# Optimization experiments

Hardware: AMD Instinct MI355X
Metric: run time of the kernel (lower is better)

The kernel has to match this reference:

```python
import jax, jax.numpy as jnp
import numpy as np
from jax import lax

B, T, D, H = 4096, 256, 18, 32


def setup_inputs() -> dict:
    key = jax.random.key(0)
    ks = jax.random.split(key, 9)
    s = 1.0 / np.sqrt(H)  # PyTorch LSTM init scale
    return {
        "batch": jax.random.normal(ks[0], (B, T, D), dtype=jnp.float32),
        "W_ih": jax.random.normal(ks[1], (4 * H, D), dtype=jnp.float32) * s,
        "W_hh": jax.random.normal(ks[2], (4 * H, H), dtype=jnp.float32) * s,
        "b_ih": jax.random.normal(ks[3], (4 * H,), dtype=jnp.float32) * s,
        "b_hh": jax.random.normal(ks[4], (4 * H,), dtype=jnp.float32) * s,
        "W1": jax.random.normal(ks[5], (512, H * T), dtype=jnp.float32) * 0.02,
        "b1": jax.random.normal(ks[6], (512,), dtype=jnp.float32) * 0.02,
        "W2": jax.random.normal(ks[7], (1, 512), dtype=jnp.float32) * 0.02,
        "b2": jax.random.normal(ks[8], (1,), dtype=jnp.float32) * 0.02,
    }


def _lstm(batch, W_ih, W_hh, b_ih, b_hh):
    b, t, _ = batch.shape
    h = batch.dtype.type
    # Precompute input projections for all timesteps: [B, T, 4H]
    x_proj = jnp.einsum('bti,gi->btg', batch, W_ih) + b_ih + b_hh
    W_hh_T = W_hh.T  # [H, 4H]

    def step(carry, xp):
        h_prev, c_prev = carry
        gates = xp + h_prev @ W_hh_T  # [B, 4H]
        i, f, g, o = jnp.split(gates, 4, axis=-1)  # PyTorch gate order i,f,g,o
        i = jax.nn.sigmoid(i)
        f = jax.nn.sigmoid(f)
        g = jnp.tanh(g)
        o = jax.nn.sigmoid(o)
        c = f * c_prev + i * g
        h_new = o * jnp.tanh(c)
        return (h_new, c), h_new

    h0 = jnp.zeros((b, H), dtype=batch.dtype)
    c0 = jnp.zeros((b, H), dtype=batch.dtype)
    _, hs = lax.scan(step, (h0, c0), x_proj.transpose(1, 0, 2))  # hs: [T, B, H]
    return hs.transpose(1, 0, 2)  # [B, T, H]


def reference(batch, W_ih, W_hh, b_ih, b_hh, W1, b1, W2, b2):
    hs = _lstm(batch, W_ih, W_hh, b_ih, b_hh)            # [B, T, H]
    flat = hs.reshape(hs.shape[0], -1)                   # [B, T*H]
    hid = jax.nn.relu(flat @ W1.T + b1)                  # [B, 512]
    return hid @ W2.T + b2                               # [B, 1]
```

## Files before the change

### kernel.cpp

```cpp
#include <hip/hip_runtime.h>
#include <hip/hip_bf16.h>
#include <stdint.h>

typedef float f32x4 __attribute__((ext_vector_type(4)));
typedef _Float16 half8 __attribute__((ext_vector_type(8)));

#define B_ 4096
#define T_ 256
#define D_ 18
#define H_ 32
#define GK 8192
#define GN 512
#define KSPLIT 4
#define SLOT 520

__device__ __forceinline__ float fsig(float x) {
  float e = __builtin_amdgcn_exp2f(-1.442695041f * x);
  return __builtin_amdgcn_rcpf(1.0f + e);
}
__device__ __forceinline__ void ldsbar() {
  asm volatile("s_waitcnt lgkmcnt(0)\n\ts_barrier" ::: "memory");
}

__global__ __launch_bounds__(256) void cvtw1_kernel(const float* __restrict__ w1,
                                                    unsigned short* __restrict__ dst) {
  int i = blockIdx.x * 256 + threadIdx.x;
  float4 v = ((const float4*)w1)[i];
  unsigned short a = __builtin_bit_cast(unsigned short, (_Float16)v.x);
  unsigned short b = __builtin_bit_cast(unsigned short, (_Float16)v.y);
  unsigned short c = __builtin_bit_cast(unsigned short, (_Float16)v.z);
  unsigned short d = __builtin_bit_cast(unsigned short, (_Float16)v.w);
  uint2 o; o.x = (unsigned)a | ((unsigned)b << 16); o.y = (unsigned)c | ((unsigned)d << 16);
  ((uint2*)dst)[i] = o;
}

__global__ __launch_bounds__(512) void lstm_kernel(
    const float* __restrict__ batch, const float* __restrict__ W_ih,
    const float* __restrict__ W_hh, const float* __restrict__ b_ih,
    const float* __restrict__ b_hh, _Float16* __restrict__ hs) {
  __shared__ _Float16 hist[16 * SLOT];
  __shared__ _Float16 xs[2 * 4096];

  const int tid = (int)threadIdx.x;
  const int lane = tid & 63;
  const int w = tid >> 6;
  const int lq = lane >> 4;
  const int lr = lane & 15;
  const int b0 = (int)blockIdx.x * 16;

  half8 wx, wh;
  {
    int grow = (lr & 3) * 32 + w * 4 + (lr >> 2);
#pragma unroll
    for (int j = 0; j < 8; ++j) {
      int k = lq * 8 + j;
      wx[j] = (k < D_) ? (_Float16)W_ih[grow * D_ + k] : (_Float16)0.0f;
      wh[j] = (_Float16)W_hh[grow * H_ + k];
    }
  }
  f32x4 bias4;
#pragma unroll
  for (int r = 0; r < 4; ++r) {
    int g = r * 32 + w * 4 + lq;
    bias4[r] = b_ih[g] + b_hh[g];
  }

  const int rdo = lr * 32 + ((lq ^ ((lr >> 1) & 3)) << 3);
  const int kcol = w * 4 + lq;
  const int wro = lr * 32 + ((((kcol >> 3) ^ ((lr >> 1) & 3))) << 3) + (kcol & 7);

  const int fe = tid >> 5;
  const int fs = (tid >> 2) & 7;
  const int fg = tid & 3;
  const int fl_rd = fs * SLOT + fe * 32 + ((fg ^ ((fe >> 1) & 3)) << 3);
  _Float16* fl_wp = hs + (size_t)(b0 + fe) * GK + fs * H_ + fg * 8;

  const int e0 = tid / 36, q0 = tid - e0 * 36;
  const int i1 = tid + 512;
  const int e1 = i1 / 36, q1 = i1 - e1 * 36;
  const float* xld0 = batch + (size_t)(b0 + e0) * (T_ * D_) + q0 * 4;
  const float* xld1 = batch + (size_t)(b0 + e1) * (T_ * D_) + q1 * 4;
  float4 xv0, xv1;

#define XLOAD(tb)                                                              \
  do {                                                                         \
    xv0 = *(const float4*)(xld0 + (tb) * 144);                                 \
    if (tid < 64) xv1 = *(const float4*)(xld1 + (tb) * 144);                   \
  } while (0)

#define XPUT(E, Q, V, buf)                                                     \
  do {                                                                         \
    int swz_ = ((E) >> 1) & 3;                                                 \
    _Pragma("unroll") for (int j = 0; j < 4; ++j) {                            \
      int f_ = (Q) * 4 + j;                                                    \
      int to_ = (f_ * 57) >> 10;                          \
      int d_ = f_ - to_ * 18;                                                  \
      float val_ = (j == 0) ? (V).x : (j == 1) ? (V).y : (j == 2) ? (V).z : (V).w; \
      xs[(buf) * 4096 + to_ * 512 + (E) * 32 + (((d_ >> 3) ^ swz_) << 3) + (d_ & 7)] = \
          (_Float16)val_;                                                      \
    }                                                                          \
  } while (0)

#define XSTORE(buf)                                                            \
  do {                                                                         \
    XPUT(e0, q0, xv0, buf);                                                    \
    if (tid < 64) XPUT(e1, q1, xv1, buf);                                      \
  } while (0)

#define STEP(tt, AXC, PRE)                                                     \
  do {                                                                         \
    _Float16* hrd = ((tt) == 0 ? po + 7 * SLOT : pr + ((tt)-1) * SLOT);        \
    half8 hf = *(const half8*)&hrd[rdo];                                       \
    f32x4 acc = __builtin_amdgcn_mfma_f32_16x16x32_f16(wh, hf, AXC, 0, 0, 0);  \
    PRE;                                                                       \
    float ei = __builtin_amdgcn_exp2f(-1.442695041f * acc[0]);                 \
    float eg = __builtin_amdgcn_exp2f(-2.885390082f * acc[2]);                 \
    float ig = (1.0f - eg) *                                                   \
               __builtin_amdgcn_rcpf((1.0f + ei) * (1.0f + eg));               \
    float fv = fsig(acc[1]);                                                   \
    c = fmaf(fv, c, ig);                                                       \
    float eo = __builtin_amdgcn_exp2f(-1.442695041f * acc[3]);                 \
    float ec = __builtin_amdgcn_exp2f(-2.885390082f * c);                      \
    float h = (1.0f - ec) *                                                    \
              __builtin_amdgcn_rcpf((1.0f + eo) * (1.0f + ec));                \
    pr[(tt)*SLOT + wro] = (_Float16)h;                                         \
    ldsbar();                                                                  \
  } while (0)

  XLOAD(0);
  for (int i = tid; i < 16 * SLOT; i += 512) hist[i] = (_Float16)0.0f;
  for (int i = tid; i < 8192; i += 512) xs[i] = (_Float16)0.0f;
  ldsbar();
  XSTORE(0);
  XLOAD(1);
  ldsbar();

  float c = 0.0f;
  for (int blk = 0; blk < 32; ++blk) {
    const int p = blk & 1;
    _Float16* pr = hist + p * (8 * SLOT);
    _Float16* po = hist + (p ^ 1) * (8 * SLOT);
    const int xo = p * 4096;

    half8 xq[8];
#pragma unroll
    for (int j = 0; j < 8; ++j) xq[j] = *(const half8*)&xs[xo + j * 512 + rdo];
    f32x4 ax0, ax1;
    ax0 = __builtin_amdgcn_mfma_f32_16x16x32_f16(wx, xq[0], bias4, 0, 0, 0);

    STEP(0, ax0, ax1 = __builtin_amdgcn_mfma_f32_16x16x32_f16(wx, xq[1], bias4, 0, 0, 0));
    STEP(1, ax1, ax0 = __builtin_amdgcn_mfma_f32_16x16x32_f16(wx, xq[2], bias4, 0, 0, 0));
    STEP(2, ax0, ax1 = __builtin_amdgcn_mfma_f32_16x16x32_f16(wx, xq[3], bias4, 0, 0, 0));
    STEP(3, ax1, ax0 = __builtin_amdgcn_mfma_f32_16x16x32_f16(wx, xq[4], bias4, 0, 0, 0));
    if (blk < 31) XSTORE(p ^ 1);
    if (blk < 30) XLOAD(blk + 2);
    STEP(4, ax0, ax1 = __builtin_amdgcn_mfma_f32_16x16x32_f16(wx, xq[5], bias4, 0, 0, 0));
    if (blk) {
      half8 hv = *(const half8*)&hist[(p ^ 1) * (8 * SLOT) + fl_rd];
      *(half8*)(fl_wp + (size_t)(blk - 1) * (8 * H_)) = hv;
    }
    STEP(5, ax1, ax0 = __builtin_amdgcn_mfma_f32_16x16x32_f16(wx, xq[6], bias4, 0, 0, 0));
    STEP(6, ax0, ax1 = __builtin_amdgcn_mfma_f32_16x16x32_f16(wx, xq[7], bias4, 0, 0, 0));
    STEP(7, ax1, );
  }
  {
    half8 hv = *(const half8*)&hist[8 * SLOT + fl_rd];
    *(half8*)(fl_wp + (size_t)31 * (8 * H_)) = hv;
  }
#undef STEP
#undef XSTORE
#undef XPUT
#undef XLOAD
}

__global__ __launch_bounds__(256, 2) void gemm_kernel(
    const _Float16* __restrict__ Ahs, const _Float16* __restrict__ Bw1,
    float* __restrict__ part) {
  __shared__ _Float16 As[2 * 128 * 64];
  __shared__ _Float16 Bs[2 * 128 * 64];

  const int bid = (int)blockIdx.x;
  const int m0 = (bid & 31) << 7;
  const int n0 = ((bid >> 5) & 3) << 7;
  const int ksp = bid >> 7;
  const int k0 = ksp << 11;
  float* outp = part + (size_t)ksp * ((size_t)B_ * GN);

  const int tid = (int)threadIdx.x;
  const int lane = tid & 63, w = tid >> 6;
  const int wm = w & 1, wn = w >> 1;
  const int lq = lane >> 4, lr = lane & 15;

  const _Float16* gA[4]; const _Float16* gB[4]; int lp[4];
#pragma unroll
  for (int j = 0; j < 4; ++j) {
    int p = tid + 256 * j;
    int row = p >> 3, q = p & 7, cg = q ^ (row & 7);
    gA[j] = Ahs + (size_t)(m0 + row) * GK + k0 + cg * 8;
    gB[j] = Bw1 + (size_t)(n0 + row) * GK + k0 + cg * 8;
    lp[j] = p * 8;
  }

  int offA[4][2], offB[4][2];
#pragma unroll
  for (int mt = 0; mt < 4; ++mt)
#pragma unroll
    for (int ks = 0; ks < 2; ++ks) {
      int m = wm * 64 + mt * 16 + lr;
      offA[mt][ks] = m * 64 + (((lq + ks * 4) ^ (m & 7)) << 3);
      int n = wn * 64 + mt * 16 + lr;
      offB[mt][ks] = n * 64 + (((lq + ks * 4) ^ (n & 7)) << 3);
    }

  f32x4 acc[4][4];
#pragma unroll
  for (int mt = 0; mt < 4; ++mt)
#pragma unroll
    for (int nt = 0; nt < 4; ++nt) {
      acc[mt][nt][0] = 0.f; acc[mt][nt][1] = 0.f;
      acc[mt][nt][2] = 0.f; acc[mt][nt][3] = 0.f;
    }

  half8 va0[4], vb0[4], va1[4], vb1[4];
#pragma unroll
  for (int j = 0; j < 4; ++j) {
    va0[j] = *(const half8*)gA[j];        vb0[j] = *(const half8*)gB[j];
    va1[j] = *(const half8*)(gA[j] + 64); vb1[j] = *(const half8*)(gB[j] + 64);
    gA[j] += 128; gB[j] += 128;
  }

#define GPHASE(SET, POFF, guard)                                               \
  do {                                                                         \
    _Pragma("unroll") for (int j = 0; j < 4; ++j) {                            \
      *(half8*)&As[(POFF) + lp[j]] = va##SET[j];                               \
      *(half8*)&Bs[(POFF) + lp[j]] = vb##SET[j];                               \
    }                                                                          \
    if (guard) {                                                               \
      _Pragma("unroll") for (int j = 0; j < 4; ++j) {                          \
        va##SET[j] = *(const half8*)gA[j];                                     \
        vb##SET[j] = *(const half8*)gB[j];                                     \
        gA[j] += 64; gB[j] += 64;                                              \
      }                                                                        \
    }                                                                          \
    ldsbar();                                                                  \
    half8 af[4][2], bf[4][2];                                                  \
    _Pragma("unroll") for (int mt = 0; mt < 4; ++mt)                           \
      _Pragma("unroll") for (int ks = 0; ks < 2; ++ks) {                       \
        af[mt][ks] = *(const half8*)&As[(POFF) + offA[mt][ks]];                \
        bf[mt][ks] = *(const half8*)&Bs[(POFF) + offB[mt][ks]];                \
      }                                                                        \
    _Pragma("unroll") for (int ks = 0; ks < 2; ++ks)                           \
      _Pragma("unroll") for (int mt = 0; mt < 4; ++mt)                         \
        _Pragma("unroll") for (int nt = 0; nt < 4; ++nt)                       \
          acc[mt][nt] = __builtin_amdgcn_mfma_f32_16x16x32_f16(                \
              af[mt][ks], bf[nt][ks], acc[mt][nt], 0, 0, 0);                   \
  } while (0)

  for (int it2 = 0; it2 < 16; ++it2) {
    const bool g = (it2 < 15);
    GPHASE(0, 0, g);
    GPHASE(1, 8192, g);
  }
#undef GPHASE

#pragma unroll
  for (int mt = 0; mt < 4; ++mt)
#pragma unroll
    for (int nt = 0; nt < 4; ++nt) {
      int n = n0 + wn * 64 + nt * 16 + lr;
#pragma unroll
      for (int r = 0; r < 4; ++r) {
        int m = m0 + wm * 64 + mt * 16 + lq * 4 + r;
        outp[(size_t)m * GN + n] = acc[mt][nt][r];
      }
    }
}

__global__ __launch_bounds__(256) void head_kernel(const float* __restrict__ part,
                                                   const float* __restrict__ b1,
                                                   const float* __restrict__ W2,
                                                   const float* __restrict__ b2,
                                                   float* __restrict__ out) {
  const int b = (int)(blockIdx.x * 4 + (threadIdx.x >> 6));
  const int l = (int)(threadIdx.x & 63);
  const size_t stride = (size_t)B_ * GN;
  const float4* b14 = (const float4*)b1;
  const float4* w4 = (const float4*)W2;
  float s = 0.0f;
#pragma unroll
  for (int p = 0; p < 2; ++p) {
    int i = p * 64 + l;
    float4 hv = ((const float4*)(part + (size_t)b * GN))[i];
#pragma unroll
    for (int sp = 1; sp < KSPLIT; ++sp) {
      float4 pv = ((const float4*)(part + sp * stride + (size_t)b * GN))[i];
      hv.x += pv.x; hv.y += pv.y; hv.z += pv.z; hv.w += pv.w;
    }
    float4 bv = b14[i], wv = w4[i];
    float t0 = fmaxf(hv.x + bv.x, 0.0f);
    float t1 = fmaxf(hv.y + bv.y, 0.0f);
    float t2 = fmaxf(hv.z + bv.z, 0.0f);
    float t3 = fmaxf(hv.w + bv.w, 0.0f);
    s = fmaf(t0, wv.x, s); s = fmaf(t1, wv.y, s);
    s = fmaf(t2, wv.z, s); s = fmaf(t3, wv.w, s);
  }
#pragma unroll
  for (int off = 32; off >= 1; off >>= 1) s += __shfl_xor(s, off);
  if (l == 0) out[b] = s + b2[0];
}

extern "C" void kernel_launch(void* const* d_in, const int* in_sizes, int n_in,
                              void* d_out, int out_size, void* d_ws, size_t ws_size,
                              hipStream_t stream) {
  const float* batch = (const float*)d_in[0];
  const float* W_ih = (const float*)d_in[1];
  const float* W_hh = (const float*)d_in[2];
  const float* b_ih = (const float*)d_in[3];
  const float* b_hh = (const float*)d_in[4];
  const float* W1 = (const float*)d_in[5];
  const float* b1 = (const float*)d_in[6];
  const float* W2 = (const float*)d_in[7];
  const float* b2 = (const float*)d_in[8];
  float* out = (float*)d_out;

  char* ws = (char*)d_ws;
  _Float16* hs = (_Float16*)ws;
  _Float16* w1h = (_Float16*)(ws + 67108864);
  float* part = (float*)(ws + 67108864 + 8388608);

  cvtw1_kernel<<<4096, 256, 0, stream>>>(W1, (unsigned short*)w1h);
  lstm_kernel<<<256, 512, 0, stream>>>(batch, W_ih, W_hh, b_ih, b_hh, hs);
  gemm_kernel<<<512, 256, 0, stream>>>(hs, w1h, part);
  head_kernel<<<1024, 256, 0, stream>>>(part, b1, W2, b2, out);
}
```

Measured before the change: 233.8 us.

## Halve LSTM block to 4 waves, each computing two hidden units per lane

The LSTM kernel now runs with 256 threads instead of 512. Each wave issues two MFMAs per step for the recurrent and input projections, so every lane holds all four gates for two hidden units. The gate math is rewritten to fold the sigmoid/tanh divisions into fewer reciprocals, and the two h values go to LDS as one packed half2 store. This shortens the per-step barrier across fewer waves and reduces transcendental work, but it doubles the serial work per lane on the recurrence critical path and leaves only four waves per CU.

```diff
diff --git a/kernel.cpp b/kernel.cpp
--- a/kernel.cpp
+++ b/kernel.cpp
@@ -4,6 +4,7 @@
 
 typedef float f32x4 __attribute__((ext_vector_type(4)));
 typedef _Float16 half8 __attribute__((ext_vector_type(8)));
+typedef _Float16 half2_ __attribute__((ext_vector_type(2)));
 
 #define B_ 4096
 #define T_ 256
@@ -14,10 +15,11 @@
 #define KSPLIT 4
 #define SLOT 520
 
-__device__ __forceinline__ float fsig(float x) {
-  float e = __builtin_amdgcn_exp2f(-1.442695041f * x);
-  return __builtin_amdgcn_rcpf(1.0f + e);
-}
+#define K1_ 1.442695041f
+#define K2_ 2.885390082f
+#define X2_ __builtin_amdgcn_exp2f
+#define RCP_ __builtin_amdgcn_rcpf
+
 __device__ __forceinline__ void ldsbar() {
   asm volatile("s_waitcnt lgkmcnt(0)\n\ts_barrier" ::: "memory");
 }
@@ -34,7 +36,7 @@
   ((uint2*)dst)[i] = o;
 }
 
-__global__ __launch_bounds__(512) void lstm_kernel(
+__global__ __launch_bounds__(256) void lstm_kernel(
     const float* __restrict__ batch, const float* __restrict__ W_ih,
     const float* __restrict__ W_hh, const float* __restrict__ b_ih,
     const float* __restrict__ b_hh, _Float16* __restrict__ hs) {
@@ -48,44 +50,57 @@
   const int lr = lane & 15;
   const int b0 = (int)blockIdx.x * 16;
 
-  half8 wx, wh;
+  half8 wx0, wx1, wh0, wh1;
   {
-    int grow = (lr & 3) * 32 + w * 4 + (lr >> 2);
+    int gq = (lr & 3) >> 1;
+    int hrow = (lr >> 2) * 8 + w * 2 + (lr & 1);
+    int g0 = (0 + gq) * 32 + hrow;
+    int g1 = (2 + gq) * 32 + hrow;
 #pragma unroll
     for (int j = 0; j < 8; ++j) {
       int k = lq * 8 + j;
-      wx[j] = (k < D_) ? (_Float16)W_ih[grow * D_ + k] : (_Float16)0.0f;
-      wh[j] = (_Float16)W_hh[grow * H_ + k];
-    }
-  }
-  f32x4 bias4;
+      wx0[j] = (k < D_) ? (_Float16)W_ih[g0 * D_ + k] : (_Float16)0.0f;
+      wx1[j] = (k < D_) ? (_Float16)W_ih[g1 * D_ + k] : (_Float16)0.0f;
+      wh0[j] = (_Float16)W_hh[g0 * H_ + k];
+      wh1[j] = (_Float16)W_hh[g1 * H_ + k];
+    }
+  }
+  f32x4 bias0, bias1;
 #pragma unroll
   for (int r = 0; r < 4; ++r) {
-    int g = r * 32 + w * 4 + lq;
-    bias4[r] = b_ih[g] + b_hh[g];
-  }
-
-  const int rdo = lr * 32 + ((lq ^ ((lr >> 1) & 3)) << 3);
-  const int kcol = w * 4 + lq;
-  const int wro = lr * 32 + ((((kcol >> 3) ^ ((lr >> 1) & 3))) << 3) + (kcol & 7);
-
-  const int fe = tid >> 5;
-  const int fs = (tid >> 2) & 7;
-  const int fg = tid & 3;
-  const int fl_rd = fs * SLOT + fe * 32 + ((fg ^ ((fe >> 1) & 3)) << 3);
-  _Float16* fl_wp = hs + (size_t)(b0 + fe) * GK + fs * H_ + fg * 8;
+    int hrow = lq * 8 + w * 2 + (r & 1);
+    int ga = (r >> 1) * 32 + hrow;
+    int gb = (2 + (r >> 1)) * 32 + hrow;
+    bias0[r] = b_ih[ga] + b_hh[ga];
+    bias1[r] = b_ih[gb] + b_hh[gb];
+  }
+
+  const int swz = (lr >> 1) & 3;
+  const int rdo = lr * 32 + ((lq ^ swz) << 3);
+  const int wro2 = rdo + w * 2;
+
+  int fl_rd[2]; _Float16* fl_wp[2];
+#pragma unroll
+  for (int u = 0; u < 2; ++u) {
+    int idx = tid + u * 256;
+    int fe = idx >> 5, fs = (idx >> 2) & 7, fg = idx & 3;
+    fl_rd[u] = fs * SLOT + fe * 32 + ((fg ^ ((fe >> 1) & 3)) << 3);
+    fl_wp[u] = hs + (size_t)(b0 + fe) * GK + fs * H_ + fg * 8;
+  }
 
   const int e0 = tid / 36, q0 = tid - e0 * 36;
-  const int i1 = tid + 512;
-  const int e1 = i1 / 36, q1 = i1 - e1 * 36;
+  const int i1 = tid + 256, e1 = i1 / 36, q1 = i1 - e1 * 36;
+  const int i2 = tid + 512, e2 = i2 / 36, q2 = i2 - e2 * 36;
   const float* xld0 = batch + (size_t)(b0 + e0) * (T_ * D_) + q0 * 4;
   const float* xld1 = batch + (size_t)(b0 + e1) * (T_ * D_) + q1 * 4;
-  float4 xv0, xv1;
+  const float* xld2 = batch + (size_t)(b0 + e2) * (T_ * D_) + q2 * 4;
+  float4 xv0, xv1, xv2;
 
 #define XLOAD(tb)                                                              \
   do {                                                                         \
     xv0 = *(const float4*)(xld0 + (tb) * 144);                                 \
-    if (tid < 64) xv1 = *(const float4*)(xld1 + (tb) * 144);                   \
+    xv1 = *(const float4*)(xld1 + (tb) * 144);                                 \
+    if (tid < 64) xv2 = *(const float4*)(xld2 + (tb) * 144);                   \
   } while (0)
 
 #define XPUT(E, Q, V, buf)                                                     \
@@ -104,68 +119,99 @@
 #define XSTORE(buf)                                                            \
   do {                                                                         \
     XPUT(e0, q0, xv0, buf);                                                    \
-    if (tid < 64) XPUT(e1, q1, xv1, buf);                                      \
-  } while (0)
-
-#define STEP(tt, AXC, PRE)                                                     \
-  do {                                                                         \
-    _Float16* hrd = ((tt) == 0 ? po + 7 * SLOT : pr + ((tt)-1) * SLOT);        \
+    XPUT(e1, q1, xv1, buf);                                                    \
+    if (tid < 64) XPUT(e2, q2, xv2, buf);                                      \
+  } while (0)
+
+#define STEP(tt, AX0, AX1, ...)                                                \
+  do {                                                                         \
+    const _Float16* hrd = ((tt) == 0 ? po + 7 * SLOT : pr + ((tt)-1) * SLOT);  \
     half8 hf = *(const half8*)&hrd[rdo];                                       \
-    f32x4 acc = __builtin_amdgcn_mfma_f32_16x16x32_f16(wh, hf, AXC, 0, 0, 0);  \
-    PRE;                                                                       \
-    float ei = __builtin_amdgcn_exp2f(-1.442695041f * acc[0]);                 \
-    float eg = __builtin_amdgcn_exp2f(-2.885390082f * acc[2]);                 \
-    float ig = (1.0f - eg) *                                                   \
-               __builtin_amdgcn_rcpf((1.0f + ei) * (1.0f + eg));               \
-    float fv = fsig(acc[1]);                                                   \
-    c = fmaf(fv, c, ig);                                                       \
-    float eo = __builtin_amdgcn_exp2f(-1.442695041f * acc[3]);                 \
-    float ec = __builtin_amdgcn_exp2f(-2.885390082f * c);                      \
-    float h = (1.0f - ec) *                                                    \
-              __builtin_amdgcn_rcpf((1.0f + eo) * (1.0f + ec));                \
-    pr[(tt)*SLOT + wro] = (_Float16)h;                                         \
+    f32x4 a0 = __builtin_amdgcn_mfma_f32_16x16x32_f16(wh0, hf, AX0, 0, 0, 0);  \
+    f32x4 a1 = __builtin_amdgcn_mfma_f32_16x16x32_f16(wh1, hf, AX1, 0, 0, 0);  \
+    __VA_ARGS__;                                                               \
+    _Float16 hp0, hp1;                                                         \
+    {                                                                          \
+      float ei = X2_(-K1_ * a0[0]); float ef = X2_(-K1_ * a0[2]);              \
+      float eg = X2_(-K2_ * a1[0]); float eo = X2_(-K1_ * a1[2]);              \
+      float pi_ = (1.0f + ei) * (1.0f + eg);                                   \
+      float num = fmaf(c0, pi_, (1.0f + ef) * (1.0f - eg));                    \
+      c0 = num * RCP_((1.0f + ef) * pi_);                                      \
+      float ec = X2_(-K2_ * c0);                                               \
+      hp0 = (_Float16)((1.0f - ec) * RCP_((1.0f + eo) * (1.0f + ec)));         \
+    }                                                                          \
+    {                                                                          \
+      float ei = X2_(-K1_ * a0[1]); float ef = X2_(-K1_ * a0[3]);              \
+      float eg = X2_(-K2_ * a1[1]); float eo = X2_(-K1_ * a1[3]);              \
+      float pi_ = (1.0f + ei) * (1.0f + eg);                                   \
+      float num = fmaf(c1, pi_, (1.0f + ef) * (1.0f - eg));                    \
+      c1 = num * RCP_((1.0f + ef) * pi_);                                      \
+      float ec = X2_(-K2_ * c1);                                               \
+      hp1 = (_Float16)((1.0f - ec) * RCP_((1.0f + eo) * (1.0f + ec)));         \
+    }                                                                          \
+    half2_ hp; hp[0] = hp0; hp[1] = hp1;                                       \
+    *(half2_*)&pr[(tt)*SLOT + wro2] = hp;                                      \
     ldsbar();                                                                  \
   } while (0)
 
   XLOAD(0);
-  for (int i = tid; i < 16 * SLOT; i += 512) hist[i] = (_Float16)0.0f;
-  for (int i = tid; i < 8192; i += 512) xs[i] = (_Float16)0.0f;
+  for (int i = tid; i < 16 * SLOT; i += 256) hist[i] = (_Float16)0.0f;
+  for (int i = tid; i < 8192; i += 256) xs[i] = (_Float16)0.0f;
   ldsbar();
   XSTORE(0);
   XLOAD(1);
   ldsbar();
 
-  float c = 0.0f;
+  float c0 = 0.0f, c1 = 0.0f;
   for (int blk = 0; blk < 32; ++blk) {
     const int p = blk & 1;
     _Float16* pr = hist + p * (8 * SLOT);
-    _Float16* po = hist + (p ^ 1) * (8 * SLOT);
+    const _Float16* po = hist + (p ^ 1) * (8 * SLOT);
     const int xo = p * 4096;
 
     half8 xq[8];
 #pragma unroll
     for (int j = 0; j < 8; ++j) xq[j] = *(const half8*)&xs[xo + j * 512 + rdo];
-    f32x4 ax0, ax1;
-    ax0 = __builtin_amdgcn_mfma_f32_16x16x32_f16(wx, xq[0], bias4, 0, 0, 0);
-
-    STEP(0, ax0, ax1 = __builtin_amdgcn_mfma_f32_16x16x32_f16(wx, xq[1], bias4, 0, 0, 0));
-    STEP(1, ax1, ax0 = __builtin_amdgcn_mfma_f32_16x16x32_f16(wx, xq[2], bias4, 0, 0, 0));
-    STEP(2, ax0, ax1 = __builtin_amdgcn_mfma_f32_16x16x32_f16(wx, xq[3], bias4, 0, 0, 0));
-    STEP(3, ax1, ax0 = __builtin_amdgcn_mfma_f32_16x16x32_f16(wx, xq[4], bias4, 0, 0, 0));
+    f32x4 axA0 = __builtin_amdgcn_mfma_f32_16x16x32_f16(wx0, xq[0], bias0, 0, 0, 0);
+    f32x4 axA1 = __builtin_amdgcn_mfma_f32_16x16x32_f16(wx1, xq[0], bias1, 0, 0, 0);
+    f32x4 axB0, axB1;
+
+    STEP(0, axA0, axA1,
+         axB0 = __builtin_amdgcn_mfma_f32_16x16x32_f16(wx0, xq[1], bias0, 0, 0, 0);
+         axB1 = __builtin_amdgcn_mfma_f32_16x16x32_f16(wx1, xq[1], bias1, 0, 0, 0));
+    STEP(1, axB0, axB1,
+         axA0 = __builtin_amdgcn_mfma_f32_16x16x32_f16(wx0, xq[2], bias0, 0, 0, 0);
+         axA1 = __builtin_amdgcn_mfma_f32_16x16x32_f16(wx1, xq[2], bias1, 0, 0, 0));
+    STEP(2, axA0, axA1,
+         axB0 = __builtin_amdgcn_mfma_f32_16x16x32_f16(wx0, xq[3], bias0, 0, 0, 0);
+         axB1 = __builtin_amdgcn_mfma_f32_16x16x32_f16(wx1, xq[3], bias1, 0, 0, 0));
+    STEP(3, axB0, axB1,
+         axA0 = __builtin_amdgcn_mfma_f32_16x16x32_f16(wx0, xq[4], bias0, 0, 0, 0);
+         axA1 = __builtin_amdgcn_mfma_f32_16x16x32_f16(wx1, xq[4], bias1, 0, 0, 0));
     if (blk < 31) XSTORE(p ^ 1);
     if (blk < 30) XLOAD(blk + 2);
-    STEP(4, ax0, ax1 = __builtin_amdgcn_mfma_f32_16x16x32_f16(wx, xq[5], bias4, 0, 0, 0));
+    STEP(4, axA0, axA1,
+         axB0 = __builtin_amdgcn_mfma_f32_16x16x32_f16(wx0, xq[5], bias0, 0, 0, 0);
+         axB1 = __builtin_amdgcn_mfma_f32_16x16x32_f16(wx1, xq[5], bias1, 0, 0, 0));
     if (blk) {
-      half8 hv = *(const half8*)&hist[(p ^ 1) * (8 * SLOT) + fl_rd];
-      *(half8*)(fl_wp + (size_t)(blk - 1) * (8 * H_)) = hv;
-    }
-    STEP(5, ax1, ax0 = __builtin_amdgcn_mfma_f32_16x16x32_f16(wx, xq[6], bias4, 0, 0, 0));
-    STEP(6, ax0, ax1 = __builtin_amdgcn_mfma_f32_16x16x32_f16(wx, xq[7], bias4, 0, 0, 0));
-    STEP(7, ax1, );
-  }
-  {
-    half8 hv = *(const half8*)&hist[8 * SLOT + fl_rd];
-    *(half8*)(fl_wp + (size_t)31 * (8 * H_)) = hv;
+#pragma unroll
+      for (int u = 0; u < 2; ++u) {
+        half8 hv = *(const half8*)&hist[(p ^ 1) * (8 * SLOT) + fl_rd[u]];
+        *(half8*)(fl_wp[u] + (size_t)(blk - 1) * (8 * H_)) = hv;
+      }
+    }
+    STEP(5, axB0, axB1,
+         axA0 = __builtin_amdgcn_mfma_f32_16x16x32_f16(wx0, xq[6], bias0, 0, 0, 0);
+         axA1 = __builtin_amdgcn_mfma_f32_16x16x32_f16(wx1, xq[6], bias1, 0, 0, 0));
+    STEP(6, axA0, axA1,
+         axB0 = __builtin_amdgcn_mfma_f32_16x16x32_f16(wx0, xq[7], bias0, 0, 0, 0);
+         axB1 = __builtin_amdgcn_mfma_f32_16x16x32_f16(wx1, xq[7], bias1, 0, 0, 0));
+    STEP(7, axB0, axB1, );
+  }
+#pragma unroll
+  for (int u = 0; u < 2; ++u) {
+    half8 hv = *(const half8*)&hist[8 * SLOT + fl_rd[u]];
+    *(half8*)(fl_wp[u] + (size_t)31 * (8 * H_)) = hv;
   }
 #undef STEP
 #undef XSTORE
@@ -329,7 +375,7 @@
   float* part = (float*)(ws + 67108864 + 8388608);
 
   cvtw1_kernel<<<4096, 256, 0, stream>>>(W1, (unsigned short*)w1h);
-  lstm_kernel<<<256, 512, 0, stream>>>(batch, W_ih, W_hh, b_ih, b_hh, hs);
+  lstm_kernel<<<256, 256, 0, stream>>>(batch, W_ih, W_hh, b_ih, b_hh, hs);
   gemm_kernel<<<512, 256, 0, stream>>>(hs, w1h, part);
   head_kernel<<<1024, 256, 0, stream>>>(part, b1, W2, b2, out);
 }
```

Result: slower. 239.6 us (+2.5%).

## Stage GEMM tiles via direct global-to-LDS loads and fuse LSTM gate reciprocals

Applied to the files above, without the earlier changes.

The GEMM main loop now loads A and B tiles with global_load_lds (async global-to-LDS DMA), double-buffered in LDS, instead of going through VGPRs and ds_write. This removes the register staging and the LDS write instructions, but each iteration now waits on a full vmcnt barrier, and a stage holds one 64-wide K slice rather than two in flight. Separately, the LSTM cell update merges the input, forget and g-gate sigmoid/tanh reciprocals into a single rcp, taking transcendental ops off the serial recurrent path.

```diff
diff --git a/kernel.cpp b/kernel.cpp
--- a/kernel.cpp
+++ b/kernel.cpp
@@ -14,12 +14,21 @@
 #define KSPLIT 4
 #define SLOT 520
 
-__device__ __forceinline__ float fsig(float x) {
-  float e = __builtin_amdgcn_exp2f(-1.442695041f * x);
-  return __builtin_amdgcn_rcpf(1.0f + e);
-}
+#define K1_ 1.442695041f
+#define K2_ 2.885390082f
+#define X2_ __builtin_amdgcn_exp2f
+#define RCP_ __builtin_amdgcn_rcpf
+
 __device__ __forceinline__ void ldsbar() {
   asm volatile("s_waitcnt lgkmcnt(0)\n\ts_barrier" ::: "memory");
+}
+__device__ __forceinline__ void fullbar() {
+  asm volatile("s_waitcnt vmcnt(0) lgkmcnt(0)\n\ts_barrier" ::: "memory");
+}
+__device__ __forceinline__ void gl_lds16(const _Float16* g, _Float16* l) {
+  __builtin_amdgcn_global_load_lds(
+      (const __attribute__((address_space(1))) unsigned int*)g,
+      (__attribute__((address_space(3))) unsigned int*)l, 16, 0, 0);
 }
 
 __global__ __launch_bounds__(256) void cvtw1_kernel(const float* __restrict__ w1,
@@ -113,16 +122,15 @@
     half8 hf = *(const half8*)&hrd[rdo];                                       \
     f32x4 acc = __builtin_amdgcn_mfma_f32_16x16x32_f16(wh, hf, AXC, 0, 0, 0);  \
     PRE;                                                                       \
-    float ei = __builtin_amdgcn_exp2f(-1.442695041f * acc[0]);                 \
-    float eg = __builtin_amdgcn_exp2f(-2.885390082f * acc[2]);                 \
-    float ig = (1.0f - eg) *                                                   \
-               __builtin_amdgcn_rcpf((1.0f + ei) * (1.0f + eg));               \
-    float fv = fsig(acc[1]);                                                   \
-    c = fmaf(fv, c, ig);                                                       \
-    float eo = __builtin_amdgcn_exp2f(-1.442695041f * acc[3]);                 \
-    float ec = __builtin_amdgcn_exp2f(-2.885390082f * c);                      \
-    float h = (1.0f - ec) *                                                    \
-              __builtin_amdgcn_rcpf((1.0f + eo) * (1.0f + ec));                \
+    float ei = X2_(-K1_ * acc[0]);                                             \
+    float ef = X2_(-K1_ * acc[1]);                                             \
+    float eg = X2_(-K2_ * acc[2]);                                             \
+    float eo = X2_(-K1_ * acc[3]);                                             \
+    float pi_ = (1.0f + ei) * (1.0f + eg);                                     \
+    float num = fmaf(c, pi_, (1.0f + ef) * (1.0f - eg));                       \
+    c = num * RCP_((1.0f + ef) * pi_);                                         \
+    float ec = X2_(-K2_ * c);                                                  \
+    float h = (1.0f - ec) * RCP_((1.0f + eo) * (1.0f + ec));                   \
     pr[(tt)*SLOT + wro] = (_Float16)h;                                         \
     ldsbar();                                                                  \
   } while (0)
@@ -191,14 +199,17 @@
   const int wm = w & 1, wn = w >> 1;
   const int lq = lane >> 4, lr = lane & 15;
 
-  const _Float16* gA[4]; const _Float16* gB[4]; int lp[4];
+  const _Float16* gA[4]; const _Float16* gB[4];
+  _Float16* lA[4]; _Float16* lB[4];
 #pragma unroll
   for (int j = 0; j < 4; ++j) {
     int p = tid + 256 * j;
     int row = p >> 3, q = p & 7, cg = q ^ (row & 7);
     gA[j] = Ahs + (size_t)(m0 + row) * GK + k0 + cg * 8;
     gB[j] = Bw1 + (size_t)(n0 + row) * GK + k0 + cg * 8;
-    lp[j] = p * 8;
+    int wbase = (w * 64 + 256 * j) * 8;
+    lA[j] = As + wbase;
+    lB[j] = Bs + wbase;
   }
 
   int offA[4][2], offB[4][2];
@@ -221,47 +232,40 @@
       acc[mt][nt][2] = 0.f; acc[mt][nt][3] = 0.f;
     }
 
-  half8 va0[4], vb0[4], va1[4], vb1[4];
-#pragma unroll
-  for (int j = 0; j < 4; ++j) {
-    va0[j] = *(const half8*)gA[j];        vb0[j] = *(const half8*)gB[j];
-    va1[j] = *(const half8*)(gA[j] + 64); vb1[j] = *(const half8*)(gB[j] + 64);
-    gA[j] += 128; gB[j] += 128;
-  }
-
-#define GPHASE(SET, POFF, guard)                                               \
+#define STAGE(POFF)                                                            \
   do {                                                                         \
     _Pragma("unroll") for (int j = 0; j < 4; ++j) {                            \
-      *(half8*)&As[(POFF) + lp[j]] = va##SET[j];                               \
-      *(half8*)&Bs[(POFF) + lp[j]] = vb##SET[j];                               \
+      gl_lds16(gA[j], lA[j] + (POFF));                                         \
+      gl_lds16(gB[j], lB[j] + (POFF));                                         \
+      gA[j] += 64; gB[j] += 64;                                                \
     }                                                                          \
-    if (guard) {                                                               \
-      _Pragma("unroll") for (int j = 0; j < 4; ++j) {                          \
-        va##SET[j] = *(const half8*)gA[j];                                     \
-        vb##SET[j] = *(const half8*)gB[j];                                     \
-        gA[j] += 64; gB[j] += 64;                                              \
-      }                                                                        \
-    }                                                                          \
-    ldsbar();                                                                  \
-    half8 af[4][2], bf[4][2];                                                  \
-    _Pragma("unroll") for (int mt = 0; mt < 4; ++mt)                           \
-      _Pragma("unroll") for (int ks = 0; ks < 2; ++ks) {                       \
-        af[mt][ks] = *(const half8*)&As[(POFF) + offA[mt][ks]];                \
-        bf[mt][ks] = *(const half8*)&Bs[(POFF) + offB[mt][ks]];                \
-      }                                                                        \
-    _Pragma("unroll") for (int ks = 0; ks < 2; ++ks)                           \
-      _Pragma("unroll") for (int mt = 0; mt < 4; ++mt)                         \
-        _Pragma("unroll") for (int nt = 0; nt < 4; ++nt)                       \
-          acc[mt][nt] = __builtin_amdgcn_mfma_f32_16x16x32_f16(                \
-              af[mt][ks], bf[nt][ks], acc[mt][nt], 0, 0, 0);                   \
-  } while (0)
-
-  for (int it2 = 0; it2 < 16; ++it2) {
-    const bool g = (it2 < 15);
-    GPHASE(0, 0, g);
-    GPHASE(1, 8192, g);
-  }
-#undef GPHASE
+  } while (0)
+
+  STAGE(0);
+  fullbar();
+
+  for (int it = 0; it < 32; ++it) {
+    const int POFF = (it & 1) * 8192;
+    if (it < 31) STAGE(POFF ^ 8192);
+    half8 af[4][2], bf[4][2];
+#pragma unroll
+    for (int mt = 0; mt < 4; ++mt)
+#pragma unroll
+      for (int ks = 0; ks < 2; ++ks) {
+        af[mt][ks] = *(const half8*)&As[POFF + offA[mt][ks]];
+        bf[mt][ks] = *(const half8*)&Bs[POFF + offB[mt][ks]];
+      }
+#pragma unroll
+    for (int ks = 0; ks < 2; ++ks)
+#pragma unroll
+      for (int mt = 0; mt < 4; ++mt)
+#pragma unroll
+        for (int nt = 0; nt < 4; ++nt)
+          acc[mt][nt] = __builtin_amdgcn_mfma_f32_16x16x32_f16(
+              af[mt][ks], bf[nt][ks], acc[mt][nt], 0, 0, 0);
+    fullbar();
+  }
+#undef STAGE
 
 #pragma unroll
   for (int mt = 0; mt < 4; ++mt)
```

Result: faster. 228.0 us (-2.5%).
